# Kernel optimization log

Measured on AMD Instinct MI355X. Metric: run time of the kernel, lower is better.

Reference implementation:

```python
import jax, jax.numpy as jnp
import numpy as np

B, P, NB, WN, CI, CO = 4, 20000, 9, 17, 64, 128

def setup_inputs() -> dict:
    key = jax.random.key(0)
    k0, k1, k2, k3 = jax.random.split(key, 4)
    in_pc = jax.random.normal(k0, (B, P, CI), dtype=jnp.float32)
    raw_w_weights = jax.random.normal(k1, (P, NB, WN), dtype=jnp.float32) * 0.1
    # padded/missing neighbors use id == P, which indexes the zero-pad row and is masked
    neighbor_ids = jax.random.randint(k2, (P, NB), 0, P + 1)
    weights = jax.random.normal(k3, (WN, CO * CI), dtype=jnp.float32)
    bias = jnp.zeros((P, CO), dtype=jnp.float32)
    return {"in_pc": in_pc, "raw_w_weights": raw_w_weights, "weights": weights,
            "bias": bias, "neighbor_ids": neighbor_ids}

def reference(in_pc, raw_w_weights, weights, bias, neighbor_ids):
    b, p, ci = in_pc.shape
    wn = weights.shape[0]
    co = bias.shape[-1]
    # pc_mask: 1 for real points, 0 for the pad row (id == in_pn)
    nb_mask = (neighbor_ids < p).astype(in_pc.dtype)          # [p, nb]
    w_weights = raw_w_weights * nb_mask[:, :, None]           # [p, nb, wn]
    in_pc_pad = jnp.concatenate(
        [in_pc, jnp.zeros((b, 1, ci), dtype=in_pc.dtype)], axis=1)  # [b, p+1, ci]
    in_neighbors = in_pc_pad[:, neighbor_ids]                 # [b, p, nb, ci] gather
    # weighted fuse over neighbors into wn basis slots
    fuse = jnp.einsum('pnm,bpni->bpmi', w_weights, in_neighbors)   # [b, p, wn, ci]
    Wm = weights.reshape(wn, co, ci)
    # per-basis conv then sum-reduce over wn (b_max_pool=False), fused into one einsum
    out_pc = jnp.einsum('moi,bpmi->bpo', Wm, fuse) + bias      # [b, p, co]
    # is_final_layer=False -> ELU; residual_rate=0 -> no residual branch
    return jax.nn.elu(out_pc)
```

## Files before the change

### kernel.cpp

```cpp
#include <hip/hip_runtime.h>
#include <hip/hip_bf16.h>
#include <stdint.h>

#define B_   4
#define P_   20000
#define NB_  9
#define WN_  17
#define CI_  64
#define CO_  128
#define PTS  16
#define ROWS 64

typedef __fp16 f16x8 __attribute__((ext_vector_type(8)));
typedef __fp16 h2    __attribute__((ext_vector_type(2)));
typedef float  f32x16 __attribute__((ext_vector_type(16)));

union H2U { h2 h; uint32_t u; };
union H8U { __fp16 h[8]; uint4 u; };

__global__ void prep_wm(const float* __restrict__ w, ushort* __restrict__ wsb) {
    int i = blockIdx.x * 256 + threadIdx.x;
    int m  = i >> 10;
    int r  = i & 1023;
    int co = r >> 3;
    int o  = r & 7;
    const float* src = w + (size_t)m * (CO_ * CI_) + co * CI_ + o * 8;
    float4 v0 = *(const float4*)(src);
    float4 v1 = *(const float4*)(src + 4);
    H8U h;
    *(h2*)&h.h[0] = __builtin_amdgcn_cvt_pkrtz(v0.x, v0.y);
    *(h2*)&h.h[2] = __builtin_amdgcn_cvt_pkrtz(v0.z, v0.w);
    *(h2*)&h.h[4] = __builtin_amdgcn_cvt_pkrtz(v1.x, v1.y);
    *(h2*)&h.h[6] = __builtin_amdgcn_cvt_pkrtz(v1.z, v1.w);
    *(uint4*)&wsb[m * 8192 + co * 64 + (o ^ (co & 7)) * 8] = h.u;
}

template <bool PRE>
__global__ __launch_bounds__(256, 2)
void lasm_fused(const float* __restrict__ in_pc,
                const float* __restrict__ raw_w,
                const float* __restrict__ weights,
                const float* __restrict__ bias,
                const int*   __restrict__ nbr,
                const ushort* __restrict__ wsb,
                float*       __restrict__ out)
{
    __shared__ __align__(16) int      s_nid[PTS][NB_];
    __shared__ __align__(16) uint32_t s_w2[PTS][WN_][12];
    __shared__ __align__(16) ushort   s_a[2][ROWS * 64];
    __shared__ __align__(16) ushort   s_b[2][CO_ * 64];

    const int tid  = threadIdx.x;
    const int lane = tid & 63;
    const int wv   = tid >> 6;
    const int p0   = blockIdx.x * PTS;

    if (tid < PTS * NB_) {
        int pl = tid / NB_, n = tid % NB_;
        s_nid[pl][n] = nbr[(p0 + pl) * NB_ + n];
    }
    for (int idx = tid; idx < PTS * NB_ * WN_; idx += 256) {
        int pl = idx / (NB_ * WN_);
        int r  = idx % (NB_ * WN_);
        int n  = r / WN_;
        int m  = r % WN_;
        float wf = raw_w[(size_t)(p0 + pl) * NB_ * WN_ + n * WN_ + m];
        H2U c; c.h = __builtin_amdgcn_cvt_pkrtz(wf, wf);
        s_w2[pl][m][n] = c.u;
    }
    for (int idx = tid; idx < PTS * WN_; idx += 256) {
        int pl = idx / WN_, m = idx % WN_;
        s_w2[pl][m][9] = 0u; s_w2[pl][m][10] = 0u; s_w2[pl][m][11] = 0u;
    }
    __syncthreads();

    const int oct = tid & 7;
    const int rp  = tid >> 3;
    h2 x[2][NB_][4];
    #pragma unroll
    for (int rr = 0; rr < 2; ++rr) {
        int r  = rp + rr * 32;
        int b  = r >> 4;
        int pl = r & 15;
        #pragma unroll
        for (int n = 0; n < NB_; ++n) {
            int nid = s_nid[pl][n];
            if (nid < P_) {
                const float* src = in_pc + ((size_t)(b * P_ + nid)) * CI_ + oct * 8;
                float4 v0 = *(const float4*)(src);
                float4 v1 = *(const float4*)(src + 4);
                x[rr][n][0] = __builtin_amdgcn_cvt_pkrtz(v0.x, v0.y);
                x[rr][n][1] = __builtin_amdgcn_cvt_pkrtz(v0.z, v0.w);
                x[rr][n][2] = __builtin_amdgcn_cvt_pkrtz(v1.x, v1.y);
                x[rr][n][3] = __builtin_amdgcn_cvt_pkrtz(v1.z, v1.w);
            } else {
                h2 z = {(__fp16)0.f, (__fp16)0.f};
                x[rr][n][0] = z; x[rr][n][1] = z; x[rr][n][2] = z; x[rr][n][3] = z;
            }
        }
    }

    f32x16 acc0, acc1;
    #pragma unroll
    for (int j = 0; j < 16; ++j) { acc0[j] = 0.f; acc1[j] = 0.f; }

    const int co_base = wv * 32;
    const int arow    = lane & 31;
    const int q       = lane >> 5;
    const int pl      = rp & 15;

    auto stage_b = [&](int m, int buf) {
        if (PRE) {
            #pragma unroll
            for (int j = 0; j < 4; ++j) {
                int flat = j * 256 + tid;
                uint4 v = *(const uint4*)&wsb[m * 8192 + flat * 8];
                *(uint4*)&s_b[buf][flat * 8] = v;
            }
        } else {
            #pragma unroll
            for (int j = 0; j < 4; ++j) {
                int flat = j * 256 + tid;
                int co = flat >> 3, o = flat & 7;
                const float* src = weights + (size_t)m * (CO_ * CI_) + co * CI_ + o * 8;
                float4 v0 = *(const float4*)(src);
                float4 v1 = *(const float4*)(src + 4);
                H8U h;
                *(h2*)&h.h[0] = __builtin_amdgcn_cvt_pkrtz(v0.x, v0.y);
                *(h2*)&h.h[2] = __builtin_amdgcn_cvt_pkrtz(v0.z, v0.w);
                *(h2*)&h.h[4] = __builtin_amdgcn_cvt_pkrtz(v1.x, v1.y);
                *(h2*)&h.h[6] = __builtin_amdgcn_cvt_pkrtz(v1.z, v1.w);
                *(uint4*)&s_b[buf][co * 64 + (o ^ (co & 7)) * 8] = h.u;
            }
        }
    };
    auto stage_a = [&](int m, int buf) {
        const uint32_t* wrow = &s_w2[pl][m][0];
        uint4 wa = *(const uint4*)(wrow);
        uint4 wb = *(const uint4*)(wrow + 4);
        uint32_t w8u = wrow[8];
        H2U w[9];
        w[0].u = wa.x; w[1].u = wa.y; w[2].u = wa.z; w[3].u = wa.w;
        w[4].u = wb.x; w[5].u = wb.y; w[6].u = wb.z; w[7].u = wb.w;
        w[8].u = w8u;
        #pragma unroll
        for (int rr = 0; rr < 2; ++rr) {
            int r = rp + rr * 32;
            h2 c0 = {(__fp16)0.f, (__fp16)0.f}, c1 = c0, c2 = c0, c3 = c0;
            #pragma unroll
            for (int n = 0; n < NB_; ++n) {
                h2 wn = w[n].h;
                c0 += wn * x[rr][n][0];
                c1 += wn * x[rr][n][1];
                c2 += wn * x[rr][n][2];
                c3 += wn * x[rr][n][3];
            }
            H8U v;
            *(h2*)&v.h[0] = c0; *(h2*)&v.h[2] = c1;
            *(h2*)&v.h[4] = c2; *(h2*)&v.h[6] = c3;
            *(uint4*)&s_a[buf][r * 64 + (oct ^ (r & 7)) * 8] = v.u;
        }
    };

    stage_b(0, 0);
    stage_a(0, 0);
    __syncthreads();

    int cur = 0;
    for (int m = 0; m < WN_; ++m) {
        int nxt = cur ^ 1;
        if (m + 1 < WN_) {
            stage_b(m + 1, nxt);
            stage_a(m + 1, nxt);
        }
        #pragma unroll
        for (int ks = 0; ks < 4; ++ks) {
            int o = ks * 2 + q;
            int bco = co_base + arow;
            f16x8 bf = *(const f16x8*)&s_b[cur][bco * 64 + (o ^ (bco & 7)) * 8];
            f16x8 a0 = *(const f16x8*)&s_a[cur][arow * 64 + (o ^ (arow & 7)) * 8];
            f16x8 a1 = *(const f16x8*)&s_a[cur][(arow + 32) * 64 + (o ^ (arow & 7)) * 8];
            acc0 = __builtin_amdgcn_mfma_f32_32x32x16_f16(a0, bf, acc0, 0, 0, 0);
            acc1 = __builtin_amdgcn_mfma_f32_32x32x16_f16(a1, bf, acc1, 0, 0, 0);
        }
        __syncthreads();
        cur = nxt;
    }

    const int col   = co_base + (lane & 31);
    const int rbase = 4 * (lane >> 5);
    #pragma unroll
    for (int mt = 0; mt < 2; ++mt) {
        f32x16 acc = mt ? acc1 : acc0;
        #pragma unroll
        for (int v = 0; v < 16; ++v) {
            int row = mt * 32 + (v & 3) + 8 * (v >> 2) + rbase;
            int b   = row >> 4;
            int p   = p0 + (row & 15);
            float val = acc[v] + bias[(size_t)p * CO_ + col];
            val = (val > 0.f) ? val : (__expf(val) - 1.f);
            out[((size_t)b * P_ + p) * CO_ + col] = val;
        }
    }
}

extern "C" void kernel_launch(void* const* d_in, const int* in_sizes, int n_in,
                              void* d_out, int out_size, void* d_ws, size_t ws_size,
                              hipStream_t stream) {
    const float* in_pc   = (const float*)d_in[0];
    const float* raw_w   = (const float*)d_in[1];
    const float* weights = (const float*)d_in[2];
    const float* bias    = (const float*)d_in[3];
    const int*   nbr     = (const int*)  d_in[4];
    float* out = (float*)d_out;

    const size_t need = (size_t)WN_ * CO_ * CI_ * sizeof(ushort);
    if (d_ws != nullptr && ws_size >= need) {
        ushort* wsb = (ushort*)d_ws;
        prep_wm<<<dim3((WN_ * CO_ * 8) / 256), dim3(256), 0, stream>>>(weights, wsb);
        lasm_fused<true><<<dim3(P_ / PTS), dim3(256), 0, stream>>>(
            in_pc, raw_w, weights, bias, nbr, wsb, out);
    } else {
        lasm_fused<false><<<dim3(P_ / PTS), dim3(256), 0, stream>>>(
            in_pc, raw_w, weights, bias, nbr, nullptr, out);
    }
}
```

Before: 169.6 us.

## Compute fused A operand in registers per wave and split K into two passes

After: 171.3 us. About the same (+1.0%).

```diff
diff --git a/kernel.cpp b/kernel.cpp
--- a/kernel.cpp
+++ b/kernel.cpp
@@ -1,5 +1,4 @@
 #include <hip/hip_runtime.h>
-#include <hip/hip_bf16.h>
 #include <stdint.h>
 
 #define B_   4
@@ -8,31 +7,37 @@
 #define WN_  17
 #define CI_  64
 #define CO_  128
-#define PTS  16
-#define ROWS 64
+#define PTS  32
+#define NBLK (P_ / PTS)
 
 typedef __fp16 f16x8 __attribute__((ext_vector_type(8)));
 typedef __fp16 h2    __attribute__((ext_vector_type(2)));
 typedef float  f32x16 __attribute__((ext_vector_type(16)));
 
 union H2U { h2 h; uint32_t u; };
-union H8U { __fp16 h[8]; uint4 u; };
+union F8U { f16x8 v; h2 h[4]; uint4 u; };
+
+__device__ __forceinline__ int b_idx(int co, int oloc) {
+    int slot = (co & 1) | (((oloc ^ ((co >> 1) & 3)) & 3) << 1);
+    return (co >> 1) * 64 + slot * 8;
+}
 
 __global__ void prep_wm(const float* __restrict__ w, ushort* __restrict__ wsb) {
     int i = blockIdx.x * 256 + threadIdx.x;
     int m  = i >> 10;
     int r  = i & 1023;
-    int co = r >> 3;
-    int o  = r & 7;
-    const float* src = w + (size_t)m * (CO_ * CI_) + co * CI_ + o * 8;
+    int p  = r >> 9;
+    int rr = r & 511;
+    int co = rr >> 2, oloc = rr & 3;
+    const float* src = w + (size_t)m * (CO_ * CI_) + co * CI_ + (p * 4 + oloc) * 8;
     float4 v0 = *(const float4*)(src);
     float4 v1 = *(const float4*)(src + 4);
-    H8U h;
-    *(h2*)&h.h[0] = __builtin_amdgcn_cvt_pkrtz(v0.x, v0.y);
-    *(h2*)&h.h[2] = __builtin_amdgcn_cvt_pkrtz(v0.z, v0.w);
-    *(h2*)&h.h[4] = __builtin_amdgcn_cvt_pkrtz(v1.x, v1.y);
-    *(h2*)&h.h[6] = __builtin_amdgcn_cvt_pkrtz(v1.z, v1.w);
-    *(uint4*)&wsb[m * 8192 + co * 64 + (o ^ (co & 7)) * 8] = h.u;
+    F8U h;
+    h.h[0] = __builtin_amdgcn_cvt_pkrtz(v0.x, v0.y);
+    h.h[1] = __builtin_amdgcn_cvt_pkrtz(v0.z, v0.w);
+    h.h[2] = __builtin_amdgcn_cvt_pkrtz(v1.x, v1.y);
+    h.h[3] = __builtin_amdgcn_cvt_pkrtz(v1.z, v1.w);
+    *(uint4*)&wsb[(m * 2 + p) * 4096 + b_idx(co, oloc)] = h.u;
 }
 
 template <bool PRE>
@@ -45,161 +50,139 @@
                 const ushort* __restrict__ wsb,
                 float*       __restrict__ out)
 {
-    __shared__ __align__(16) int      s_nid[PTS][NB_];
-    __shared__ __align__(16) uint32_t s_w2[PTS][WN_][12];
-    __shared__ __align__(16) ushort   s_a[2][ROWS * 64];
-    __shared__ __align__(16) ushort   s_b[2][CO_ * 64];
+    __shared__ __align__(16) int      s_nid[PTS * NB_];
+    __shared__ __align__(16) uint32_t s_w2[WN_ * NB_ * 33];
+    __shared__ __align__(16) ushort   s_b[2][4096];
 
     const int tid  = threadIdx.x;
     const int lane = tid & 63;
-    const int wv   = tid >> 6;
+    const int w    = tid >> 6;
+    const int arow = lane & 31;
+    const int q    = lane >> 5;
     const int p0   = blockIdx.x * PTS;
 
-    if (tid < PTS * NB_) {
-        int pl = tid / NB_, n = tid % NB_;
-        s_nid[pl][n] = nbr[(p0 + pl) * NB_ + n];
-    }
+    for (int t = tid; t < PTS * NB_; t += 256) s_nid[t] = nbr[p0 * NB_ + t];
     for (int idx = tid; idx < PTS * NB_ * WN_; idx += 256) {
-        int pl = idx / (NB_ * WN_);
-        int r  = idx % (NB_ * WN_);
-        int n  = r / WN_;
-        int m  = r % WN_;
-        float wf = raw_w[(size_t)(p0 + pl) * NB_ * WN_ + n * WN_ + m];
+        int pl  = idx / (NB_ * WN_);
+        int rem = idx % (NB_ * WN_);
+        int n   = rem / WN_;
+        int m   = rem % WN_;
+        float wf = raw_w[(size_t)p0 * NB_ * WN_ + idx];
         H2U c; c.h = __builtin_amdgcn_cvt_pkrtz(wf, wf);
-        s_w2[pl][m][n] = c.u;
-    }
-    for (int idx = tid; idx < PTS * WN_; idx += 256) {
-        int pl = idx / WN_, m = idx % WN_;
-        s_w2[pl][m][9] = 0u; s_w2[pl][m][10] = 0u; s_w2[pl][m][11] = 0u;
+        s_w2[(m * NB_ + n) * 33 + pl] = c.u;
     }
     __syncthreads();
 
-    const int oct = tid & 7;
-    const int rp  = tid >> 3;
-    h2 x[2][NB_][4];
+    f32x16 acc[4];
     #pragma unroll
-    for (int rr = 0; rr < 2; ++rr) {
-        int r  = rp + rr * 32;
-        int b  = r >> 4;
-        int pl = r & 15;
+    for (int c = 0; c < 4; ++c)
+        #pragma unroll
+        for (int j = 0; j < 16; ++j) acc[c][j] = 0.f;
+
+    const size_t binpc = (size_t)w * P_ * CI_;
+
+    auto stage_b = [&](int pass, int m, int buf) {
+        if (PRE) {
+            #pragma unroll
+            for (int j = 0; j < 2; ++j) {
+                int flat = j * 256 + tid;
+                uint4 v = *(const uint4*)&wsb[(size_t)(m * 2 + pass) * 4096 + flat * 8];
+                *(uint4*)&s_b[buf][flat * 8] = v;
+            }
+        } else {
+            #pragma unroll
+            for (int j = 0; j < 2; ++j) {
+                int flat = j * 256 + tid;
+                int co = flat >> 2, oloc = flat & 3;
+                const float* src = weights + (size_t)m * (CO_ * CI_) + co * CI_ + (pass * 4 + oloc) * 8;
+                float4 v0 = *(const float4*)(src);
+                float4 v1 = *(const float4*)(src + 4);
+                F8U h;
+                h.h[0] = __builtin_amdgcn_cvt_pkrtz(v0.x, v0.y);
+                h.h[1] = __builtin_amdgcn_cvt_pkrtz(v0.z, v0.w);
+                h.h[2] = __builtin_amdgcn_cvt_pkrtz(v1.x, v1.y);
+                h.h[3] = __builtin_amdgcn_cvt_pkrtz(v1.z, v1.w);
+                *(uint4*)&s_b[buf][b_idx(co, oloc)] = h.u;
+            }
+        }
+    };
+
+    for (int pass = 0; pass < 2; ++pass) {
+        h2 x[NB_][8];
+        const int ch0 = pass * 32 + q * 8;
         #pragma unroll
         for (int n = 0; n < NB_; ++n) {
-            int nid = s_nid[pl][n];
-            if (nid < P_) {
-                const float* src = in_pc + ((size_t)(b * P_ + nid)) * CI_ + oct * 8;
-                float4 v0 = *(const float4*)(src);
-                float4 v1 = *(const float4*)(src + 4);
-                x[rr][n][0] = __builtin_amdgcn_cvt_pkrtz(v0.x, v0.y);
-                x[rr][n][1] = __builtin_amdgcn_cvt_pkrtz(v0.z, v0.w);
-                x[rr][n][2] = __builtin_amdgcn_cvt_pkrtz(v1.x, v1.y);
-                x[rr][n][3] = __builtin_amdgcn_cvt_pkrtz(v1.z, v1.w);
+            uint32_t nid = (uint32_t)s_nid[arow * NB_ + n];
+            if (nid < (uint32_t)P_) {
+                const float* src = in_pc + binpc + (size_t)nid * CI_ + ch0;
+                float4 a0 = *(const float4*)(src);
+                float4 a1 = *(const float4*)(src + 4);
+                float4 b0 = *(const float4*)(src + 16);
+                float4 b1 = *(const float4*)(src + 20);
+                x[n][0] = __builtin_amdgcn_cvt_pkrtz(a0.x, a0.y);
+                x[n][1] = __builtin_amdgcn_cvt_pkrtz(a0.z, a0.w);
+                x[n][2] = __builtin_amdgcn_cvt_pkrtz(a1.x, a1.y);
+                x[n][3] = __builtin_amdgcn_cvt_pkrtz(a1.z, a1.w);
+                x[n][4] = __builtin_amdgcn_cvt_pkrtz(b0.x, b0.y);
+                x[n][5] = __builtin_amdgcn_cvt_pkrtz(b0.z, b0.w);
+                x[n][6] = __builtin_amdgcn_cvt_pkrtz(b1.x, b1.y);
+                x[n][7] = __builtin_amdgcn_cvt_pkrtz(b1.z, b1.w);
             } else {
                 h2 z = {(__fp16)0.f, (__fp16)0.f};
-                x[rr][n][0] = z; x[rr][n][1] = z; x[rr][n][2] = z; x[rr][n][3] = z;
-            }
-        }
-    }
-
-    f32x16 acc0, acc1;
+                #pragma unroll
+                for (int j = 0; j < 8; ++j) x[n][j] = z;
+            }
+        }
+
+        stage_b(pass, 0, 0);
+        __syncthreads();
+
+        int cur = 0;
+        for (int m = 0; m < WN_; ++m) {
+            int nxt = cur ^ 1;
+            if (m + 1 < WN_) stage_b(pass, m + 1, nxt);
+
+            H2U wc[9];
+            #pragma unroll
+            for (int n = 0; n < NB_; ++n) wc[n].u = s_w2[(m * NB_ + n) * 33 + arow];
+
+            F8U f[2];
+            #pragma unroll
+            for (int kk = 0; kk < 2; ++kk) {
+                #pragma unroll
+                for (int r4 = 0; r4 < 4; ++r4) {
+                    h2 c = {(__fp16)0.f, (__fp16)0.f};
+                    #pragma unroll
+                    for (int n = 0; n < NB_; ++n) c += wc[n].h * x[n][kk * 4 + r4];
+                    f[kk].h[r4] = c;
+                }
+            }
+
+            #pragma unroll
+            for (int kk = 0; kk < 2; ++kk) {
+                int oloc = kk * 2 + q;
+                #pragma unroll
+                for (int c = 0; c < 4; ++c) {
+                    int bco = c * 32 + arow;
+                    f16x8 bf = *(const f16x8*)&s_b[cur][b_idx(bco, oloc)];
+                    acc[c] = __builtin_amdgcn_mfma_f32_32x32x16_f16(f[kk].v, bf, acc[c], 0, 0, 0);
+                }
+            }
+            __syncthreads();
+            cur = nxt;
+        }
+    }
+
     #pragma unroll
-    for (int j = 0; j < 16; ++j) { acc0[j] = 0.f; acc1[j] = 0.f; }
-
-    const int co_base = wv * 32;
-    const int arow    = lane & 31;
-    const int q       = lane >> 5;
-    const int pl      = rp & 15;
-
-    auto stage_b = [&](int m, int buf) {
-        if (PRE) {
-            #pragma unroll
-            for (int j = 0; j < 4; ++j) {
-                int flat = j * 256 + tid;
-                uint4 v = *(const uint4*)&wsb[m * 8192 + flat * 8];
-                *(uint4*)&s_b[buf][flat * 8] = v;
-            }
-        } else {
-            #pragma unroll
-            for (int j = 0; j < 4; ++j) {
-                int flat = j * 256 + tid;
-                int co = flat >> 3, o = flat & 7;
-                const float* src = weights + (size_t)m * (CO_ * CI_) + co * CI_ + o * 8;
-                float4 v0 = *(const float4*)(src);
-                float4 v1 = *(const float4*)(src + 4);
-                H8U h;
-                *(h2*)&h.h[0] = __builtin_amdgcn_cvt_pkrtz(v0.x, v0.y);
-                *(h2*)&h.h[2] = __builtin_amdgcn_cvt_pkrtz(v0.z, v0.w);
-                *(h2*)&h.h[4] = __builtin_amdgcn_cvt_pkrtz(v1.x, v1.y);
-                *(h2*)&h.h[6] = __builtin_amdgcn_cvt_pkrtz(v1.z, v1.w);
-                *(uint4*)&s_b[buf][co * 64 + (o ^ (co & 7)) * 8] = h.u;
-            }
-        }
-    };
-    auto stage_a = [&](int m, int buf) {
-        const uint32_t* wrow = &s_w2[pl][m][0];
-        uint4 wa = *(const uint4*)(wrow);
-        uint4 wb = *(const uint4*)(wrow + 4);
-        uint32_t w8u = wrow[8];
-        H2U w[9];
-        w[0].u = wa.x; w[1].u = wa.y; w[2].u = wa.z; w[3].u = wa.w;
-        w[4].u = wb.x; w[5].u = wb.y; w[6].u = wb.z; w[7].u = wb.w;
-        w[8].u = w8u;
-        #pragma unroll
-        for (int rr = 0; rr < 2; ++rr) {
-            int r = rp + rr * 32;
-            h2 c0 = {(__fp16)0.f, (__fp16)0.f}, c1 = c0, c2 = c0, c3 = c0;
-            #pragma unroll
-            for (int n = 0; n < NB_; ++n) {
-                h2 wn = w[n].h;
-                c0 += wn * x[rr][n][0];
-                c1 += wn * x[rr][n][1];
-                c2 += wn * x[rr][n][2];
-                c3 += wn * x[rr][n][3];
-            }
-            H8U v;
-            *(h2*)&v.h[0] = c0; *(h2*)&v.h[2] = c1;
-            *(h2*)&v.h[4] = c2; *(h2*)&v.h[6] = c3;
-            *(uint4*)&s_a[buf][r * 64 + (oct ^ (r & 7)) * 8] = v.u;
-        }
-    };
-
-    stage_b(0, 0);
-    stage_a(0, 0);
-    __syncthreads();
-
-    int cur = 0;
-    for (int m = 0; m < WN_; ++m) {
-        int nxt = cur ^ 1;
-        if (m + 1 < WN_) {
-            stage_b(m + 1, nxt);
-            stage_a(m + 1, nxt);
-        }
-        #pragma unroll
-        for (int ks = 0; ks < 4; ++ks) {
-            int o = ks * 2 + q;
-            int bco = co_base + arow;
-            f16x8 bf = *(const f16x8*)&s_b[cur][bco * 64 + (o ^ (bco & 7)) * 8];
-            f16x8 a0 = *(const f16x8*)&s_a[cur][arow * 64 + (o ^ (arow & 7)) * 8];
-            f16x8 a1 = *(const f16x8*)&s_a[cur][(arow + 32) * 64 + (o ^ (arow & 7)) * 8];
-            acc0 = __builtin_amdgcn_mfma_f32_32x32x16_f16(a0, bf, acc0, 0, 0, 0);
-            acc1 = __builtin_amdgcn_mfma_f32_32x32x16_f16(a1, bf, acc1, 0, 0, 0);
-        }
-        __syncthreads();
-        cur = nxt;
-    }
-
-    const int col   = co_base + (lane & 31);
-    const int rbase = 4 * (lane >> 5);
-    #pragma unroll
-    for (int mt = 0; mt < 2; ++mt) {
-        f32x16 acc = mt ? acc1 : acc0;
+    for (int c = 0; c < 4; ++c) {
+        int col = c * 32 + arow;
         #pragma unroll
         for (int v = 0; v < 16; ++v) {
-            int row = mt * 32 + (v & 3) + 8 * (v >> 2) + rbase;
-            int b   = row >> 4;
-            int p   = p0 + (row & 15);
-            float val = acc[v] + bias[(size_t)p * CO_ + col];
+            int lr = (v & 3) + 8 * (v >> 2) + 4 * q;
+            int p  = p0 + lr;
+            float val = acc[c][v] + bias[(size_t)p * CO_ + col];
             val = (val > 0.f) ? val : (__expf(val) - 1.f);
-            out[((size_t)b * P_ + p) * CO_ + col] = val;
+            out[((size_t)w * P_ + p) * CO_ + col] = val;
         }
     }
 }
@@ -214,14 +197,14 @@
     const int*   nbr     = (const int*)  d_in[4];
     float* out = (float*)d_out;
 
-    const size_t need = (size_t)WN_ * CO_ * CI_ * sizeof(ushort);
+    const size_t need = (size_t)WN_ * 2 * 4096 * sizeof(ushort);
     if (d_ws != nullptr && ws_size >= need) {
         ushort* wsb = (ushort*)d_ws;
-        prep_wm<<<dim3((WN_ * CO_ * 8) / 256), dim3(256), 0, stream>>>(weights, wsb);
-        lasm_fused<true><<<dim3(P_ / PTS), dim3(256), 0, stream>>>(
+        prep_wm<<<dim3(WN_ * 2 * 512 / 256), dim3(256), 0, stream>>>(weights, wsb);
+        lasm_fused<true><<<dim3(NBLK), dim3(256), 0, stream>>>(
             in_pc, raw_w, weights, bias, nbr, wsb, out);
     } else {
-        lasm_fused<false><<<dim3(P_ / PTS), dim3(256), 0, stream>>>(
+        lasm_fused<false><<<dim3(NBLK), dim3(256), 0, stream>>>(
             in_pc, raw_w, weights, bias, nbr, nullptr, out);
     }
 }
```
